# Performance work log

Hardware: AMD Instinct MI355X
Metric: run time of the kernel (lower is better)

Reference implementation:

```python
import jax, jax.numpy as jnp
import numpy as np

BT, N = 4, 2048
FIN, FOUT = 512, 128          # GGE in/out; FOUT == PPI output (GAGA constraint)
PIN, POUT = 256, 128          # PPIGE in/out
HEAD = 4
K = POUT // HEAD              # per-head dim = 32
NEG_SLOPE = 0.2
MASK_VAL = -1e30


def setup_inputs() -> dict:
    key = jax.random.key(0)
    ks = jax.random.split(key, 24)
    s = 0.05
    inp = {}
    inp["a"] = jax.random.normal(ks[0], (BT, FIN), jnp.float32)
    inp["bio_a"] = jax.random.normal(ks[1], (BT, N, PIN), jnp.float32)
    inp["A"] = jax.random.randint(ks[2], (BT, N, N), 0, 2, jnp.int32)
    inp["b"] = jax.random.normal(ks[3], (BT, FIN), jnp.float32)
    inp["bio_b"] = jax.random.normal(ks[4], (BT, N, PIN), jnp.float32)
    inp["B"] = jax.random.randint(ks[5], (BT, N, N), 0, 2, jnp.int32)
    # PPIGE_GAT params (shared across both graph branches)
    inp["initW"] = jax.random.normal(ks[6], (POUT, PIN), jnp.float32) * s
    inp["initb"] = jnp.zeros((POUT,), jnp.float32)
    inp["projW"] = jax.random.normal(ks[7], (POUT, POUT), jnp.float32) * s  # no bias
    inp["attw"] = jax.random.normal(ks[8], (HEAD, 2 * K), jnp.float32) * s  # per-head [2k]->1
    inp["attb"] = jnp.zeros((HEAD,), jnp.float32)
    # GGE params
    inp["ggeW1"] = jax.random.normal(ks[9], (128, FIN), jnp.float32) * s
    inp["ggeb1"] = jnp.zeros((128,), jnp.float32)
    inp["ggeW2"] = jax.random.normal(ks[10], (FOUT, 128), jnp.float32) * s
    inp["ggeb2"] = jnp.zeros((FOUT,), jnp.float32)
    # LED params (hidden = FOUT)
    inp["convW"] = jax.random.normal(ks[11], (2 * FOUT, 2 * FOUT), jnp.float32) * s  # k=1 conv
    inp["convb"] = jnp.zeros((2 * FOUT,), jnp.float32)
    inp["ledW1"] = jax.random.normal(ks[12], (FOUT, 4 * FOUT), jnp.float32) * s
    inp["ledb1"] = jnp.zeros((FOUT,), jnp.float32)
    inp["ledW2"] = jax.random.normal(ks[13], (2, FOUT), jnp.float32) * s
    inp["ledb2"] = jnp.zeros((2,), jnp.float32)
    return inp


def _gat_layer(x, adj_mask, projW, attw, attb):
    # x: [B,N,POUT]; adj_mask: [B,N,N] bool
    Bt, n, _ = x.shape
    xh = (x @ projW.T).reshape(Bt, n, HEAD, K).transpose(0, 2, 1, 3)  # [B,h,N,k]
    # score(i,j) = leaky_relu(w1.x_i + w2.x_j + b)  (equivalent to Linear on concat)
    s1 = jnp.einsum('bhnk,hk->bhn', xh, attw[:, :K])
    s2 = jnp.einsum('bhnk,hk->bhn', xh, attw[:, K:])
    scores = jax.nn.leaky_relu(
        s1[..., :, None] + s2[..., None, :] + attb[None, :, None, None], NEG_SLOPE)
    scores = jnp.where(adj_mask[:, None], scores, MASK_VAL)
    att = jax.nn.softmax(scores, axis=-1)                     # [B,h,N,N]
    out = jax.nn.relu(att @ xh)                               # [B,h,N,k]
    return out.transpose(0, 2, 1, 3).reshape(Bt, n, HEAD * K)


def _ppige(bio, adj, initW, initb, projW, attw, attb):
    x = bio @ initW.T + initb
    return _gat_layer(x, adj > 0, projW, attw, attb) + x      # residual; dropout=eval


def _gge(a, W1, b1, W2, b2):
    h = jax.nn.relu(a @ W1.T + b1)
    return jax.nn.relu(h @ W2.T + b2)


def _gaga(G, h):
    # G: [B,N,D], h: [B,D]
    att = jax.nn.softmax(jnp.einsum('bnd,bd->bn', G, h), axis=-1)
    return jnp.einsum('bnd,bn->bd', G, att)


def _led(ea, eb, convW, convb, W1, b1, W2, b2):
    # pointwise conv over the length-2 stack [ea, eb], then maxpool over length
    cnn = jnp.maximum(ea @ convW.T + convb, eb @ convW.T + convb)  # [B,2D]
    x = jax.nn.relu(jnp.concatenate([cnn, ea - eb], axis=1) @ W1.T + b1)
    return x @ W2.T + b2


def reference(a, bio_a, A, b, bio_b, B,
              initW, initb, projW, attw, attb,
              ggeW1, ggeb1, ggeW2, ggeb2,
              convW, convb, ledW1, ledb1, ledW2, ledb2):
    G_a = _ppige(bio_a, A, initW, initb, projW, attw, attb)
    G_b = _ppige(bio_b, B, initW, initb, projW, attw, attb)
    h_a = _gge(a, ggeW1, ggeb1, ggeW2, ggeb2)
    h_b = _gge(b, ggeW1, ggeb1, ggeW2, ggeb2)
    e_a = jnp.concatenate([h_a, _gaga(G_a, h_a)], axis=-1)
    e_b = jnp.concatenate([h_b, _gaga(G_b, h_b)], axis=-1)
    logits = _led(e_a, e_b, convW, convb, ledW1, ledb1, ledW2, ledb2)
    return jax.nn.log_softmax(logits, axis=-1)
```

## Files before the change

kernel.cpp:

```cpp
#include <hip/hip_runtime.h>
#include <hip/hip_bf16.h>
#include <math.h>

#define NN 2048
#define NEG 0.2f
#define LOG2E 1.44269504f

typedef short bf16x8 __attribute__((ext_vector_type(8)));
typedef float f32x16 __attribute__((ext_vector_type(16)));

__device__ __forceinline__ float dot4(float4 a, float4 b) {
  return a.x * b.x + a.y * b.y + a.z * b.z + a.w * b.w;
}

__device__ __forceinline__ unsigned short bfbits(float f) {
  union { __hip_bfloat16 b; unsigned short u; } c;
  c.b = __float2bfloat16(f);
  return c.u;
}

__global__ __launch_bounds__(256) void k12_fused(const float* __restrict__ bioA,
                                                 const float* __restrict__ bioB,
                                                 const float* __restrict__ initW,
                                                 const float* __restrict__ initb,
                                                 const float* __restrict__ projW,
                                                 const float* __restrict__ attw,
                                                 float* __restrict__ xout,
                                                 unsigned short* __restrict__ xhT2,
                                                 float* __restrict__ s1,
                                                 float* __restrict__ s2) {
  __shared__ float As[32][36];
  __shared__ float Ws[32][132];
  __shared__ float xT[128][36];
  const int t = threadIdx.x;
  const int m0 = blockIdx.x * 32;
  const float* A = (m0 < 8192) ? bioA : bioB;
  const int arow0 = (m0 < 8192) ? m0 : (m0 - 8192);
  const int og = t & 31, ig = t >> 5;

  float acc[4][4] = {};
  for (int kt = 0; kt < 256; kt += 32) {
    __syncthreads();
    {
      const int r = t >> 3, kq = t & 7;
      const float4 v = *(const float4*)&A[(arow0 + r) * 256 + kt + kq * 4];
      As[kq * 4 + 0][r] = v.x; As[kq * 4 + 1][r] = v.y;
      As[kq * 4 + 2][r] = v.z; As[kq * 4 + 3][r] = v.w;
    }
#pragma unroll
    for (int u = 0; u < 4; ++u) {
      const int f = u * 256 + t;
      const int o = f >> 3, kq = f & 7;
      const float4 v = *(const float4*)&initW[o * 256 + kt + kq * 4];
      Ws[kq * 4 + 0][o] = v.x; Ws[kq * 4 + 1][o] = v.y;
      Ws[kq * 4 + 2][o] = v.z; Ws[kq * 4 + 3][o] = v.w;
    }
    __syncthreads();
#pragma unroll
    for (int kk = 0; kk < 32; ++kk) {
      const float4 a4 = *(const float4*)&As[kk][ig * 4];
      const float4 w4 = *(const float4*)&Ws[kk][og * 4];
      const float av[4] = {a4.x, a4.y, a4.z, a4.w};
      const float wv[4] = {w4.x, w4.y, w4.z, w4.w};
#pragma unroll
      for (int ii = 0; ii < 4; ++ii)
#pragma unroll
        for (int jj = 0; jj < 4; ++jj) acc[ii][jj] += av[ii] * wv[jj];
    }
  }
  {
    const float4 b4 = *(const float4*)&initb[og * 4];
    const float bj[4] = {b4.x, b4.y, b4.z, b4.w};
#pragma unroll
    for (int ii = 0; ii < 4; ++ii) {
      const int row = m0 + ig * 4 + ii;
      float4 o4;
      o4.x = acc[ii][0] + bj[0]; o4.y = acc[ii][1] + bj[1];
      o4.z = acc[ii][2] + bj[2]; o4.w = acc[ii][3] + bj[3];
      *(float4*)&xout[row * 128 + og * 4] = o4;
    }
#pragma unroll
    for (int jj = 0; jj < 4; ++jj) {
      float4 v;
      v.x = acc[0][jj] + bj[jj]; v.y = acc[1][jj] + bj[jj];
      v.z = acc[2][jj] + bj[jj]; v.w = acc[3][jj] + bj[jj];
      *(float4*)&xT[og * 4 + jj][ig * 4] = v;
    }
  }
  __syncthreads();

  float acc2[4][4] = {};
  for (int kt = 0; kt < 128; kt += 32) {
    __syncthreads();
#pragma unroll
    for (int u = 0; u < 4; ++u) {
      const int f = u * 256 + t;
      const int o = f >> 3, kq = f & 7;
      const float4 v = *(const float4*)&projW[o * 128 + kt + kq * 4];
      Ws[kq * 4 + 0][o] = v.x; Ws[kq * 4 + 1][o] = v.y;
      Ws[kq * 4 + 2][o] = v.z; Ws[kq * 4 + 3][o] = v.w;
    }
    __syncthreads();
#pragma unroll
    for (int kk = 0; kk < 32; ++kk) {
      const float4 a4 = *(const float4*)&xT[kt + kk][ig * 4];
      const float4 w4 = *(const float4*)&Ws[kk][og * 4];
      const float av[4] = {a4.x, a4.y, a4.z, a4.w};
      const float wv[4] = {w4.x, w4.y, w4.z, w4.w};
#pragma unroll
      for (int ii = 0; ii < 4; ++ii)
#pragma unroll
        for (int jj = 0; jj < 4; ++jj) acc2[ii][jj] += av[ii] * wv[jj];
    }
  }
  const int h = og >> 3;
  const int k4i = (og & 7) * 4;
  const int g = m0 >> 13;
  const int bb = (m0 >> 11) & 3;
  const int gb = g * 4 + bb;
  const int n0 = (m0 & 2047) + ig * 4;
  const float4 w1 = *(const float4*)&attw[h * 64 + k4i];
  const float4 w2 = *(const float4*)&attw[h * 64 + 32 + k4i];
  float p1[4], p2[4];
#pragma unroll
  for (int ii = 0; ii < 4; ++ii) {
    float4 v;
    v.x = acc2[ii][0]; v.y = acc2[ii][1]; v.z = acc2[ii][2]; v.w = acc2[ii][3];
    p1[ii] = dot4(v, w1);
    p2[ii] = dot4(v, w2);
  }
  {
    const int mtile = n0 >> 4, jslot = (n0 >> 3) & 1, j8 = n0 & 7;
    const int base2 = ((((gb * 4 + h) * 128 + mtile) * 2 + jslot) * 32) * 8 + j8;
#pragma unroll
    for (int jj = 0; jj < 4; ++jj) {
      const int kin = k4i + jj;
      ushort4 u;
      u.x = bfbits(acc2[0][jj]); u.y = bfbits(acc2[1][jj]);
      u.z = bfbits(acc2[2][jj]); u.w = bfbits(acc2[3][jj]);
      *(ushort4*)&xhT2[base2 + kin * 8] = u;
    }
  }
#pragma unroll
  for (int s = 1; s < 8; s <<= 1) {
#pragma unroll
    for (int ii = 0; ii < 4; ++ii) {
      p1[ii] += __shfl_xor(p1[ii], s);
      p2[ii] += __shfl_xor(p2[ii], s);
    }
  }
  if ((og & 7) == 0) {
#pragma unroll
    for (int ii = 0; ii < 4; ++ii) {
      s1[(gb * 4 + h) * NN + n0 + ii] = p1[ii];
      s2[(gb * 4 + h) * NN + n0 + ii] = p2[ii];
    }
  }
}

#define K3_PROLOGUE                                                           \
  {                                                                           \
    const float* s2g = s2w + gb * 4 * NN;                                     \
    _Pragma("unroll")                                                         \
    for (int u = 0; u < 4; ++u) {                                             \
      const int idx = u * 2048 + t * 4;                                       \
      float4 v = *(const float4*)&s2g[idx];                                   \
      v.x *= LOG2E; v.y *= LOG2E; v.z *= LOG2E; v.w *= LOG2E;                 \
      *(float4*)&s2L[idx] = v;                                                \
    }                                                                         \
  }                                                                           \
  _Pragma("unroll")                                                           \
  for (int r4 = 0; r4 < 4; ++r4) {                                            \
    const int r = wave * 4 + r4;                                              \
    const int* arow = adj + r * NN;                                           \
    int av[32];                                                               \
    _Pragma("unroll")                                                         \
    for (int w = 0; w < 32; ++w) av[w] = __builtin_nontemporal_load(&arow[w * 64 + lane]); \
    _Pragma("unroll")                                                         \
    for (int w = 0; w < 32; ++w) {                                            \
      const unsigned long long mm = __ballot(av[w] > 0);                      \
      if (lane < 2) adjL[r * 66 + 2 * w + lane] = (unsigned int)(mm >> (32 * lane)); \
    }                                                                         \
  }

#define K3_SCORE_BODY(MM)                                                     \
    const int j0 = jlo + 16 * (MM) + jslot * 8;                               \
    const unsigned int wbits = adjL[i * 66 + ((jlo + 16 * (MM)) >> 5)];       \
    const unsigned int bits8 = wbits >> ((((MM) & 1) * 16) + jslot * 8);      \
    const float4 s2a = *(const float4*)&s2L[h * 2048 + j0];                   \
    const float4 s2b = *(const float4*)&s2L[h * 2048 + j0 + 4];               \
    const float sv[8] = {s2a.x, s2a.y, s2a.z, s2a.w,                          \
                         s2b.x, s2b.y, s2b.z, s2b.w};                         \
    union { bf16x8 v; unsigned short u[8]; } af;                              \
    float dsum = 0.f;                                                         \
    _Pragma("unroll")                                                         \
    for (int e = 0; e < 8; ++e) {                                             \
      float s = sc1v + sv[e];                                                 \
      s = fmaxf(s, NEG * s);                                                  \
      float pe = __builtin_amdgcn_exp2f(s);                                   \
      pe = ((bits8 >> e) & 1u) ? pe : 0.f;                                    \
      af.u[e] = bfbits(pe);                                                   \
      dsum += pe;                                                             \
    }                                                                         \
    den += dsum;

__global__ __launch_bounds__(512) void k3_attn(const unsigned short* __restrict__ xhT2,
                                               const float* __restrict__ s1w,
                                               const float* __restrict__ s2w,
                                               const int* __restrict__ adjA,
                                               const int* __restrict__ adjB,
                                               const float* __restrict__ attb,
                                               const float* __restrict__ x,
                                               float* __restrict__ G) {
  __shared__ __align__(16) unsigned char smem3[42240];
  unsigned int* adjL = (unsigned int*)smem3;
  float* s2L = (float*)(smem3 + 8448);
  float* denR = (float*)(smem3 + 41216);
  float* accR = (float*)smem3;

  const int t = threadIdx.x;
  const int wave = t >> 6, lane = t & 63;
  const int p = (int)blockIdx.x;
  const int blk = (p & 7) * 64 + (p >> 3);
  const int g = blk >> 8, b = (blk >> 6) & 3;
  const int i0 = (blk & 63) * 32;
  const int gb = g * 4 + b;
  const int* adj = (g ? adjB : adjA) + (b * NN + i0) * NN;
  K3_PROLOGUE
  __syncthreads();

  const int h = wave & 3;
  const int jhalf = wave >> 2;
  const int jlo = jhalf * 1024;
  const int i = lane & 31;
  const int jslot = lane >> 5;
  const float sc1v = (s1w[(gb * 4 + h) * NN + i0 + i] + attb[h]) * LOG2E;
  const unsigned short* bbase = xhT2 + (gb * 4 + h) * 65536 + jhalf * 32768 + lane * 8;
  f32x16 acc = {0.f, 0.f, 0.f, 0.f, 0.f, 0.f, 0.f, 0.f,
                0.f, 0.f, 0.f, 0.f, 0.f, 0.f, 0.f, 0.f};
  float den = 0.f;

#define K3_CSTEP(RB, MM)                                                      \
  {                                                                           \
    K3_SCORE_BODY(MM)                                                         \
    acc = __builtin_amdgcn_mfma_f32_32x32x16_bf16(af.v, RB, acc, 0, 0, 0);    \
  }

  bf16x8 fa0 = *(const bf16x8*)&bbase[0 * 512];
  bf16x8 fa1 = *(const bf16x8*)&bbase[1 * 512];
  bf16x8 fa2 = *(const bf16x8*)&bbase[2 * 512];
  bf16x8 fa3 = *(const bf16x8*)&bbase[3 * 512];
  bf16x8 fb0 = *(const bf16x8*)&bbase[4 * 512];
  bf16x8 fb1 = *(const bf16x8*)&bbase[5 * 512];
  bf16x8 fb2 = *(const bf16x8*)&bbase[6 * 512];
  bf16x8 fb3 = *(const bf16x8*)&bbase[7 * 512];
  bf16x8 fc0 = *(const bf16x8*)&bbase[8 * 512];
  bf16x8 fc1 = *(const bf16x8*)&bbase[9 * 512];
  bf16x8 fc2 = *(const bf16x8*)&bbase[10 * 512];
  bf16x8 fc3 = *(const bf16x8*)&bbase[11 * 512];
  bf16x8 fd0 = *(const bf16x8*)&bbase[12 * 512];
  bf16x8 fd1 = *(const bf16x8*)&bbase[13 * 512];
  bf16x8 fd2 = *(const bf16x8*)&bbase[14 * 512];
  bf16x8 fd3 = *(const bf16x8*)&bbase[15 * 512];
  __builtin_amdgcn_sched_barrier(0);
  for (int mb = 0; mb < 64; mb += 16) {
    K3_CSTEP(fa0, mb + 0)
    K3_CSTEP(fa1, mb + 1)
    K3_CSTEP(fa2, mb + 2)
    K3_CSTEP(fa3, mb + 3)
    __builtin_amdgcn_sched_barrier(0);
    if (mb < 48) {
      fa0 = *(const bf16x8*)&bbase[(mb + 16) * 512];
      fa1 = *(const bf16x8*)&bbase[(mb + 17) * 512];
      fa2 = *(const bf16x8*)&bbase[(mb + 18) * 512];
      fa3 = *(const bf16x8*)&bbase[(mb + 19) * 512];
    }
    __builtin_amdgcn_sched_barrier(0);
    K3_CSTEP(fb0, mb + 4)
    K3_CSTEP(fb1, mb + 5)
    K3_CSTEP(fb2, mb + 6)
    K3_CSTEP(fb3, mb + 7)
    __builtin_amdgcn_sched_barrier(0);
    if (mb < 48) {
      fb0 = *(const bf16x8*)&bbase[(mb + 20) * 512];
      fb1 = *(const bf16x8*)&bbase[(mb + 21) * 512];
      fb2 = *(const bf16x8*)&bbase[(mb + 22) * 512];
      fb3 = *(const bf16x8*)&bbase[(mb + 23) * 512];
    }
    __builtin_amdgcn_sched_barrier(0);
    K3_CSTEP(fc0, mb + 8)
    K3_CSTEP(fc1, mb + 9)
    K3_CSTEP(fc2, mb + 10)
    K3_CSTEP(fc3, mb + 11)
    __builtin_amdgcn_sched_barrier(0);
    if (mb < 48) {
      fc0 = *(const bf16x8*)&bbase[(mb + 24) * 512];
      fc1 = *(const bf16x8*)&bbase[(mb + 25) * 512];
      fc2 = *(const bf16x8*)&bbase[(mb + 26) * 512];
      fc3 = *(const bf16x8*)&bbase[(mb + 27) * 512];
    }
    __builtin_amdgcn_sched_barrier(0);
    K3_CSTEP(fd0, mb + 12)
    K3_CSTEP(fd1, mb + 13)
    K3_CSTEP(fd2, mb + 14)
    K3_CSTEP(fd3, mb + 15)
    __builtin_amdgcn_sched_barrier(0);
    if (mb < 48) {
      fd0 = *(const bf16x8*)&bbase[(mb + 28) * 512];
      fd1 = *(const bf16x8*)&bbase[(mb + 29) * 512];
      fd2 = *(const bf16x8*)&bbase[(mb + 30) * 512];
      fd3 = *(const bf16x8*)&bbase[(mb + 31) * 512];
    }
    __builtin_amdgcn_sched_barrier(0);
  }
#undef K3_CSTEP

  den += __shfl_xor(den, 32);
  if (lane < 32) denR[(h * 2 + jhalf) * 32 + lane] = den;
  __syncthreads();
  if (jhalf == 1) {
#pragma unroll
    for (int r = 0; r < 16; ++r) accR[(h * 16 + r) * 65 + lane] = acc[r];
  }
  __syncthreads();
  if (jhalf == 0) {
#pragma unroll
    for (int r = 0; r < 16; ++r) {
      const int row = (r & 3) + 8 * (r >> 2) + 4 * jslot;
      const float dinv = 1.f / (denR[(h * 2 + 0) * 32 + row] + denR[(h * 2 + 1) * 32 + row]);
      const int off = (gb * NN + i0 + row) * 128 + h * 32 + i;
      const float av2 = acc[r] + accR[(h * 16 + r) * 65 + lane];
      G[off] = fmaxf(av2 * dinv, 0.f) + x[off];
    }
  }
}

__global__ __launch_bounds__(256) void k4h_gge(const float* __restrict__ a_in,
                                               const float* __restrict__ b_in,
                                               const float* __restrict__ ggeW1,
                                               const float* __restrict__ ggeb1,
                                               const float* __restrict__ ggeW2,
                                               const float* __restrict__ ggeb2,
                                               float* __restrict__ hvbuf,
                                               float* __restrict__ e) {
  __shared__ float inL[512];
  __shared__ float h1L[128];
  const int t = threadIdx.x;
  const int wave = t >> 6, lane = t & 63;
  const int g = blockIdx.x >> 2, b = blockIdx.x & 3;
  const int gb2 = g * 4 + b;
  const float* inp = (g ? b_in : a_in) + b * 512;
  if (t < 128) *(float4*)&inL[t * 4] = *(const float4*)&inp[t * 4];
  __syncthreads();
  for (int p = 0; p < 16; ++p) {
    const int o0 = p * 8 + wave * 2;
    const float* w0 = &ggeW1[o0 * 512 + lane * 8];
    const float* w1 = &ggeW1[(o0 + 1) * 512 + lane * 8];
    const float4 i0v = *(const float4*)&inL[lane * 8];
    const float4 i1v = *(const float4*)&inL[lane * 8 + 4];
    float s0 = dot4(*(const float4*)&w0[0], i0v) + dot4(*(const float4*)&w0[4], i1v);
    float s1v = dot4(*(const float4*)&w1[0], i0v) + dot4(*(const float4*)&w1[4], i1v);
#pragma unroll
    for (int s = 1; s < 64; s <<= 1) { s0 += __shfl_xor(s0, s); s1v += __shfl_xor(s1v, s); }
    if (lane == 0) {
      h1L[o0] = fmaxf(s0 + ggeb1[o0], 0.f);
      h1L[o0 + 1] = fmaxf(s1v + ggeb1[o0 + 1], 0.f);
    }
  }
  __syncthreads();
  for (int p = 0; p < 16; ++p) {
    const int o0 = p * 8 + wave * 2;
    const float2 w0 = *(const float2*)&ggeW2[o0 * 128 + lane * 2];
    const float2 w1 = *(const float2*)&ggeW2[(o0 + 1) * 128 + lane * 2];
    const float2 hvv = *(const float2*)&h1L[lane * 2];
    float s0 = w0.x * hvv.x + w0.y * hvv.y;
    float s1v = w1.x * hvv.x + w1.y * hvv.y;
#pragma unroll
    for (int s = 1; s < 64; s <<= 1) { s0 += __shfl_xor(s0, s); s1v += __shfl_xor(s1v, s); }
    if (lane == 0) {
      const float v0 = fmaxf(s0 + ggeb2[o0], 0.f);
      const float v1 = fmaxf(s1v + ggeb2[o0 + 1], 0.f);
      hvbuf[gb2 * 128 + o0] = v0;
      hvbuf[gb2 * 128 + o0 + 1] = v1;
      e[gb2 * 256 + o0] = v0;
      e[gb2 * 256 + o0 + 1] = v1;
    }
  }
}

__global__ __launch_bounds__(256) void k4a_logits(const float* __restrict__ G,
                                                  const float* __restrict__ hv,
                                                  float* __restrict__ lg) {
  const int t = threadIdx.x;
  const int wave = t >> 6, lane = t & 63;
  const int gb = blockIdx.x >> 4, chunk = blockIdx.x & 15;
  const float2 hvv = *(const float2*)&hv[gb * 128 + lane * 2];
  const float* Gb = G + gb * NN * 128;
  const int nbase = chunk * 128 + wave * 32;
  for (int q = 0; q < 32; ++q) {
    const int n = nbase + q;
    const float2 gv = *(const float2*)&Gb[n * 128 + lane * 2];
    float part = gv.x * hvv.x + gv.y * hvv.y;
#pragma unroll
    for (int s = 1; s < 64; s <<= 1) part += __shfl_xor(part, s);
    if (lane == 0) lg[gb * NN + n] = part;
  }
}

__global__ __launch_bounds__(256) void k4b_reduce(const float* __restrict__ lg,
                                                  float* __restrict__ mz) {
  __shared__ float red[256];
  const int t = threadIdx.x;
  const int gb = blockIdx.x;
  const float* l = lg + gb * NN;
  float m = -1e30f;
  for (int n = t; n < NN; n += 256) m = fmaxf(m, l[n]);
  red[t] = m; __syncthreads();
#pragma unroll
  for (int s = 128; s > 0; s >>= 1) {
    if (t < s) red[t] = fmaxf(red[t], red[t + s]);
    __syncthreads();
  }
  const float mx = red[0]; __syncthreads();
  float z = 0.f;
  for (int n = t; n < NN; n += 256) z += __expf(l[n] - mx);
  red[t] = z; __syncthreads();
#pragma unroll
  for (int s = 128; s > 0; s >>= 1) {
    if (t < s) red[t] += red[t + s];
    __syncthreads();
  }
  if (t == 0) { mz[gb * 2] = mx; mz[gb * 2 + 1] = red[0]; }
}

__global__ __launch_bounds__(256) void k4c_wsum(const float* __restrict__ G,
                                                const float* __restrict__ lg,
                                                const float* __restrict__ mz,
                                                float* __restrict__ wsum) {
  __shared__ float pL[128];
  __shared__ float red[2][128];
  const int t = threadIdx.x;
  const int gb = blockIdx.x >> 4, chunk = blockIdx.x & 15;
  const float mx = mz[gb * 2];
  if (t < 128) pL[t] = __expf(lg[gb * NN + chunk * 128 + t] - mx);
  __syncthreads();
  const int d = t & 127, half = t >> 7;
  const float* Gb = G + (gb * NN + chunk * 128 + half * 64) * 128;
  float acc = 0.f;
  for (int q = 0; q < 64; ++q) acc += pL[half * 64 + q] * Gb[q * 128 + d];
  red[half][d] = acc;
  __syncthreads();
  if (t < 128) wsum[(gb * 16 + chunk) * 128 + t] = red[0][t] + red[1][t];
}

__global__ __launch_bounds__(256) void k5_led(const float* __restrict__ e,
                                              const float* __restrict__ wsum,
                                              const float* __restrict__ mz,
                                              const float* __restrict__ convW,
                                              const float* __restrict__ convb,
                                              const float* __restrict__ ledW1,
                                              const float* __restrict__ ledb1,
                                              const float* __restrict__ ledW2,
                                              const float* __restrict__ ledb2,
                                              float* __restrict__ out) {
  __shared__ float eaL[256], ebL[256], uL[512], xL[128], lgL[2];
  const int t = threadIdx.x;
  const int wave = t >> 6, lane = t & 63;
  const int bt = blockIdx.x;
  const int gba = bt, gbb = 4 + bt;
  if (t < 128) {
    eaL[t] = e[gba * 256 + t];
    ebL[t] = e[gbb * 256 + t];
    float sa = 0.f, sb = 0.f;
#pragma unroll
    for (int c = 0; c < 16; ++c) {
      sa += wsum[(gba * 16 + c) * 128 + t];
      sb += wsum[(gbb * 16 + c) * 128 + t];
    }
    eaL[128 + t] = sa / mz[gba * 2 + 1];
    ebL[128 + t] = sb / mz[gbb * 2 + 1];
  }
  __syncthreads();
  uL[256 + t] = eaL[t] - ebL[t];
  const float4 ea4 = *(const float4*)&eaL[lane * 4];
  const float4 eb4 = *(const float4*)&ebL[lane * 4];
  for (int p = 0; p < 32; ++p) {
    const int o0 = p * 8 + wave * 2;
    const float4 w0 = *(const float4*)&convW[o0 * 256 + lane * 4];
    const float4 w1 = *(const float4*)&convW[(o0 + 1) * 256 + lane * 4];
    float sa0 = dot4(w0, ea4), sb0 = dot4(w0, eb4);
    float sa1 = dot4(w1, ea4), sb1 = dot4(w1, eb4);
#pragma unroll
    for (int s = 1; s < 64; s <<= 1) {
      sa0 += __shfl_xor(sa0, s); sb0 += __shfl_xor(sb0, s);
      sa1 += __shfl_xor(sa1, s); sb1 += __shfl_xor(sb1, s);
    }
    if (lane == 0) {
      const float c0 = convb[o0], c1 = convb[o0 + 1];
      uL[o0] = fmaxf(sa0 + c0, sb0 + c0);
      uL[o0 + 1] = fmaxf(sa1 + c1, sb1 + c1);
    }
  }
  __syncthreads();
  for (int p = 0; p < 16; ++p) {
    const int o0 = p * 8 + wave * 2;
    const float* w0 = &ledW1[o0 * 512 + lane * 8];
    const float* w1 = &ledW1[(o0 + 1) * 512 + lane * 8];
    const float4 u0 = *(const float4*)&uL[lane * 8];
    const float4 u1 = *(const float4*)&uL[lane * 8 + 4];
    float s0 = dot4(*(const float4*)&w0[0], u0) + dot4(*(const float4*)&w0[4], u1);
    float s1v = dot4(*(const float4*)&w1[0], u0) + dot4(*(const float4*)&w1[4], u1);
#pragma unroll
    for (int s = 1; s < 64; s <<= 1) { s0 += __shfl_xor(s0, s); s1v += __shfl_xor(s1v, s); }
    if (lane == 0) {
      xL[o0] = fmaxf(s0 + ledb1[o0], 0.f);
      xL[o0 + 1] = fmaxf(s1v + ledb1[o0 + 1], 0.f);
    }
  }
  __syncthreads();
  if (wave < 2) {
    const float2 w = *(const float2*)&ledW2[wave * 128 + lane * 2];
    const float2 xv = *(const float2*)&xL[lane * 2];
    float s0 = w.x * xv.x + w.y * xv.y;
#pragma unroll
    for (int s = 1; s < 64; s <<= 1) s0 += __shfl_xor(s0, s);
    if (lane == 0) lgL[wave] = s0 + ledb2[wave];
  }
  __syncthreads();
  if (t == 0) {
    const float l0 = lgL[0], l1 = lgL[1];
    const float m = fmaxf(l0, l1);
    const float za = __expf(l0 - m) + __expf(l1 - m);
    const float lz = __logf(za);
    out[bt * 2 + 0] = l0 - m - lz;
    out[bt * 2 + 1] = l1 - m - lz;
  }
}

extern "C" void kernel_launch(void* const* d_in, const int* in_sizes, int n_in,
                              void* d_out, int out_size, void* d_ws, size_t ws_size,
                              hipStream_t stream) {
  (void)in_sizes; (void)n_in; (void)out_size; (void)ws_size;
  const float* a     = (const float*)d_in[0];
  const float* bioA  = (const float*)d_in[1];
  const int*   A     = (const int*)d_in[2];
  const float* b     = (const float*)d_in[3];
  const float* bioB  = (const float*)d_in[4];
  const int*   B     = (const int*)d_in[5];
  const float* initW = (const float*)d_in[6];
  const float* initb = (const float*)d_in[7];
  const float* projW = (const float*)d_in[8];
  const float* attw  = (const float*)d_in[9];
  const float* attb  = (const float*)d_in[10];
  const float* ggeW1 = (const float*)d_in[11];
  const float* ggeb1 = (const float*)d_in[12];
  const float* ggeW2 = (const float*)d_in[13];
  const float* ggeb2 = (const float*)d_in[14];
  const float* convW = (const float*)d_in[15];
  const float* convb = (const float*)d_in[16];
  const float* ledW1 = (const float*)d_in[17];
  const float* ledb1 = (const float*)d_in[18];
  const float* ledW2 = (const float*)d_in[19];
  const float* ledb2 = (const float*)d_in[20];

  float* ws = (float*)d_ws;
  float*          x    = ws;
  unsigned short* xhT2 = (unsigned short*)(ws + 2097152);
  float*          s1   = ws + 3145728;
  float*          s2   = ws + 3211264;
  float*          G    = ws + 3276800;
  float*          lg   = ws + 5373952;
  float*          wsum = ws + 5390336;
  float*          mz   = ws + 5406720;
  float*          hv   = ws + 5406736;
  float*          e    = ws + 5407760;
  float* out = (float*)d_out;

  k12_fused<<<512, 256, 0, stream>>>(bioA, bioB, initW, initb, projW, attw,
                                     x, xhT2, s1, s2);
  k3_attn<<<512, 512, 0, stream>>>(xhT2, s1, s2, A, B, attb, x, G);
  k4h_gge<<<8, 256, 0, stream>>>(a, b, ggeW1, ggeb1, ggeW2, ggeb2, hv, e);
  k4a_logits<<<128, 256, 0, stream>>>(G, hv, lg);
  k4b_reduce<<<8, 256, 0, stream>>>(lg, mz);
  k4c_wsum<<<128, 256, 0, stream>>>(G, lg, mz, wsum);
  k5_led<<<4, 256, 0, stream>>>(e, wsum, mz, convW, convb, ledW1, ledb1,
                                ledW2, ledb2, out);
}
```

Before: 186.4 us.

## Fuse GAGA softmax kernels into one chunked online-softmax pass

Replaces the three GAGA kernels (logits, global max/sum reduce, weighted sum) with a single kernel. Each block computes its chunk's logits, a local max and sum, and a locally weighted sum of G, and writes per-chunk partials. The LED kernel then rescales the chunk partials flash-softmax style to get the global softmax-weighted sum. This removes two launches and one extra read of the logits and of G, in exchange for some extra exp work in the final kernel.

```diff
diff --git a/kernel.cpp b/kernel.cpp
--- a/kernel.cpp
+++ b/kernel.cpp
@@ -388,74 +388,67 @@
   }
 }
 
-__global__ __launch_bounds__(256) void k4a_logits(const float* __restrict__ G,
-                                                  const float* __restrict__ hv,
-                                                  float* __restrict__ lg) {
+__global__ __launch_bounds__(256) void k4a_gaga(const float* __restrict__ G,
+                                                const float* __restrict__ hv,
+                                                float* __restrict__ wsumC,
+                                                float* __restrict__ mzC) {
+  __shared__ float lgL[128];
+  __shared__ float pL[128];
+  __shared__ float red[256];
+  __shared__ float red2[2][128];
   const int t = threadIdx.x;
   const int wave = t >> 6, lane = t & 63;
   const int gb = blockIdx.x >> 4, chunk = blockIdx.x & 15;
   const float2 hvv = *(const float2*)&hv[gb * 128 + lane * 2];
-  const float* Gb = G + gb * NN * 128;
-  const int nbase = chunk * 128 + wave * 32;
+  const float* Gb = G + (gb * NN + chunk * 128) * 128;
+  const int nbase = wave * 32;
   for (int q = 0; q < 32; ++q) {
     const int n = nbase + q;
     const float2 gv = *(const float2*)&Gb[n * 128 + lane * 2];
     float part = gv.x * hvv.x + gv.y * hvv.y;
 #pragma unroll
     for (int s = 1; s < 64; s <<= 1) part += __shfl_xor(part, s);
-    if (lane == 0) lg[gb * NN + n] = part;
-  }
-}
-
-__global__ __launch_bounds__(256) void k4b_reduce(const float* __restrict__ lg,
-                                                  float* __restrict__ mz) {
-  __shared__ float red[256];
-  const int t = threadIdx.x;
-  const int gb = blockIdx.x;
-  const float* l = lg + gb * NN;
-  float m = -1e30f;
-  for (int n = t; n < NN; n += 256) m = fmaxf(m, l[n]);
-  red[t] = m; __syncthreads();
+    if (lane == 0) lgL[n] = part;
+  }
+  __syncthreads();
+  red[t] = (t < 128) ? lgL[t] : -1e30f;
+  __syncthreads();
 #pragma unroll
   for (int s = 128; s > 0; s >>= 1) {
     if (t < s) red[t] = fmaxf(red[t], red[t + s]);
     __syncthreads();
   }
-  const float mx = red[0]; __syncthreads();
-  float z = 0.f;
-  for (int n = t; n < NN; n += 256) z += __expf(l[n] - mx);
-  red[t] = z; __syncthreads();
+  const float mc = red[0];
+  __syncthreads();
+  if (t < 128) {
+    const float pv = __expf(lgL[t] - mc);
+    pL[t] = pv;
+    red[t] = pv;
+  } else red[t] = 0.f;
+  __syncthreads();
 #pragma unroll
   for (int s = 128; s > 0; s >>= 1) {
     if (t < s) red[t] += red[t + s];
     __syncthreads();
   }
-  if (t == 0) { mz[gb * 2] = mx; mz[gb * 2 + 1] = red[0]; }
-}
-
-__global__ __launch_bounds__(256) void k4c_wsum(const float* __restrict__ G,
-                                                const float* __restrict__ lg,
-                                                const float* __restrict__ mz,
-                                                float* __restrict__ wsum) {
-  __shared__ float pL[128];
-  __shared__ float red[2][128];
-  const int t = threadIdx.x;
-  const int gb = blockIdx.x >> 4, chunk = blockIdx.x & 15;
-  const float mx = mz[gb * 2];
-  if (t < 128) pL[t] = __expf(lg[gb * NN + chunk * 128 + t] - mx);
+  const float zc = red[0];
   __syncthreads();
   const int d = t & 127, half = t >> 7;
-  const float* Gb = G + (gb * NN + chunk * 128 + half * 64) * 128;
+  const float* Gh = Gb + (half * 64) * 128;
   float acc = 0.f;
-  for (int q = 0; q < 64; ++q) acc += pL[half * 64 + q] * Gb[q * 128 + d];
-  red[half][d] = acc;
-  __syncthreads();
-  if (t < 128) wsum[(gb * 16 + chunk) * 128 + t] = red[0][t] + red[1][t];
+  for (int q = 0; q < 64; ++q) acc += pL[half * 64 + q] * Gh[q * 128 + d];
+  red2[half][d] = acc;
+  __syncthreads();
+  if (t < 128) wsumC[(gb * 16 + chunk) * 128 + t] = red2[0][t] + red2[1][t];
+  if (t == 0) {
+    mzC[(gb * 16 + chunk) * 2 + 0] = mc;
+    mzC[(gb * 16 + chunk) * 2 + 1] = zc;
+  }
 }
 
 __global__ __launch_bounds__(256) void k5_led(const float* __restrict__ e,
-                                              const float* __restrict__ wsum,
-                                              const float* __restrict__ mz,
+                                              const float* __restrict__ wsumC,
+                                              const float* __restrict__ mzC,
                                               const float* __restrict__ convW,
                                               const float* __restrict__ convb,
                                               const float* __restrict__ ledW1,
@@ -471,14 +464,24 @@
   if (t < 128) {
     eaL[t] = e[gba * 256 + t];
     ebL[t] = e[gbb * 256 + t];
-    float sa = 0.f, sb = 0.f;
+    float ma = -1e30f, mb2 = -1e30f;
 #pragma unroll
     for (int c = 0; c < 16; ++c) {
-      sa += wsum[(gba * 16 + c) * 128 + t];
-      sb += wsum[(gbb * 16 + c) * 128 + t];
-    }
-    eaL[128 + t] = sa / mz[gba * 2 + 1];
-    ebL[128 + t] = sb / mz[gbb * 2 + 1];
+      ma = fmaxf(ma, mzC[(gba * 16 + c) * 2]);
+      mb2 = fmaxf(mb2, mzC[(gbb * 16 + c) * 2]);
+    }
+    float Za = 0.f, Zb = 0.f, sa = 0.f, sb = 0.f;
+#pragma unroll
+    for (int c = 0; c < 16; ++c) {
+      const float wa = __expf(mzC[(gba * 16 + c) * 2] - ma);
+      const float wb = __expf(mzC[(gbb * 16 + c) * 2] - mb2);
+      Za += mzC[(gba * 16 + c) * 2 + 1] * wa;
+      Zb += mzC[(gbb * 16 + c) * 2 + 1] * wb;
+      sa += wsumC[(gba * 16 + c) * 128 + t] * wa;
+      sb += wsumC[(gbb * 16 + c) * 128 + t] * wb;
+    }
+    eaL[128 + t] = sa / Za;
+    ebL[128 + t] = sb / Zb;
   }
   __syncthreads();
   uL[256 + t] = eaL[t] - ebL[t];
@@ -564,25 +567,22 @@
   const float* ledb2 = (const float*)d_in[20];
 
   float* ws = (float*)d_ws;
-  float*          x    = ws;
-  unsigned short* xhT2 = (unsigned short*)(ws + 2097152);
-  float*          s1   = ws + 3145728;
-  float*          s2   = ws + 3211264;
-  float*          G    = ws + 3276800;
-  float*          lg   = ws + 5373952;
-  float*          wsum = ws + 5390336;
-  float*          mz   = ws + 5406720;
-  float*          hv   = ws + 5406736;
-  float*          e    = ws + 5407760;
+  float*          x     = ws;
+  unsigned short* xhT2  = (unsigned short*)(ws + 2097152);
+  float*          s1    = ws + 3145728;
+  float*          s2    = ws + 3211264;
+  float*          G     = ws + 3276800;
+  float*          mzC   = ws + 5373952;
+  float*          wsumC = ws + 5390336;
+  float*          hv    = ws + 5406736;
+  float*          e     = ws + 5407760;
   float* out = (float*)d_out;
 
   k12_fused<<<512, 256, 0, stream>>>(bioA, bioB, initW, initb, projW, attw,
                                      x, xhT2, s1, s2);
   k3_attn<<<512, 512, 0, stream>>>(xhT2, s1, s2, A, B, attb, x, G);
   k4h_gge<<<8, 256, 0, stream>>>(a, b, ggeW1, ggeb1, ggeW2, ggeb2, hv, e);
-  k4a_logits<<<128, 256, 0, stream>>>(G, hv, lg);
-  k4b_reduce<<<8, 256, 0, stream>>>(lg, mz);
-  k4c_wsum<<<128, 256, 0, stream>>>(G, lg, mz, wsum);
-  k5_led<<<4, 256, 0, stream>>>(e, wsum, mz, convW, convb, ledW1, ledb1,
+  k4a_gaga<<<128, 256, 0, stream>>>(G, hv, wsumC, mzC);
+  k5_led<<<4, 256, 0, stream>>>(e, wsumC, mzC, convW, convb, ledW1, ledb1,
                                 ledW2, ledb2, out);
 }
```

New measurement: 182.4 us. -2.2%, faster.
